# Kernel tuning notes

Hardware: AMD Instinct MI355X
Metric: run time of the kernel (lower is better)

The kernel has to match this reference:

```python
import jax, jax.numpy as jnp
import numpy as np

B, L, E, H, V, DT, C = 64, 80, 256, 256, 30000, 100, 4
D = 4 * L * H  # BatchNorm / FC feature dim = max_length * hidden * 4
EPS = 1e-5


def setup_inputs() -> dict:
    key = jax.random.key(0)
    ks = jax.random.split(key, 20)
    n = lambda k, shape, s: jax.random.normal(k, shape, jnp.float32) * s
    g = 1.0 / np.sqrt(H)  # pytorch LSTM init scale
    return {
        "arg1": jax.random.randint(ks[0], (B, L), 0, V, dtype=jnp.int32),
        "arg2": jax.random.randint(ks[1], (B, L), 0, V, dtype=jnp.int32),
        "seq_lengths": jnp.full((B,), L, dtype=jnp.int32),
        "transE1": jax.random.normal(ks[2], (L, DT), jnp.float32),
        "transE2": jax.random.normal(ks[3], (L, DT), jnp.float32),
        # learned parameters
        "table": n(ks[4], (V, E), 0.05),                 # embedding (xavier-ish)
        "Wih_f": n(ks[5], (4 * H, E), g),
        "Whh_f": n(ks[6], (4 * H, H), g),
        "bih_f": n(ks[7], (4 * H,), g),
        "bhh_f": n(ks[8], (4 * H,), g),
        "Wih_b": n(ks[9], (4 * H, E), g),
        "Whh_b": n(ks[10], (4 * H, H), g),
        "bih_b": n(ks[11], (4 * H,), g),
        "bhh_b": n(ks[12], (4 * H,), g),
        "R": jax.random.uniform(ks[13], (2 * E, 2 * E), jnp.float32),  # torch.rand init
        "gamma": jnp.ones((D,), jnp.float32),
        "beta": jnp.zeros((D,), jnp.float32),
        "fcW": n(ks[14], (C, D), 0.01),
        "fcb": jnp.zeros((C,), jnp.float32),
    }


def _lstm_dir(x, Wih, Whh, b):
    # x: (B, L, E); pytorch gate order i, f, g, o
    xg = jnp.einsum('ble,ge->blg', x, Wih) + b          # (B, L, 4H)
    xg = jnp.swapaxes(xg, 0, 1)                         # (L, B, 4H)
    h0 = jnp.zeros((x.shape[0], Whh.shape[1]), x.dtype)

    def step(carry, g_t):
        h, c = carry
        gates = g_t + h @ Whh.T
        i, f, gg, o = jnp.split(gates, 4, axis=-1)
        c = jax.nn.sigmoid(f) * c + jax.nn.sigmoid(i) * jnp.tanh(gg)
        h = jax.nn.sigmoid(o) * jnp.tanh(c)
        return (h, c), h

    _, hs = jax.lax.scan(step, (h0, h0), xg)
    return jnp.swapaxes(hs, 0, 1)                       # (B, L, H)


def _bilstm(x, Wih_f, Whh_f, bih_f, bhh_f, Wih_b, Whh_b, bih_b, bhh_b):
    fwd = _lstm_dir(x, Wih_f, Whh_f, bih_f + bhh_f)
    bwd = _lstm_dir(x[:, ::-1], Wih_b, Whh_b, bih_b + bhh_b)[:, ::-1]
    return jnp.concatenate([fwd, bwd], axis=-1)         # (B, L, 2H)


def _forward(arg1, arg2, transE1, transE2, table, Wih_f, Whh_f, bih_f, bhh_f,
             Wih_b, Whh_b, bih_b, bhh_b, R, gamma, beta, fcW, fcb):
    # deal_transE: relation[i,j] = tanh(mean(arg1_word_i - arg2_word_j));
    # identical for every batch element -> block-diagonal kron.
    m1 = transE1.mean(axis=1)                           # (L,)
    m2 = transE2.mean(axis=1)                           # (L,)
    rel = jnp.tanh(m1[:, None] - m2[None, :])           # (L, L)
    kg = jax.lax.stop_gradient(jnp.kron(jnp.eye(B, dtype=rel.dtype), rel))  # (B*L, B*L)

    e1 = table[arg1]                                    # (B, L, E); dropout p=0 -> identity
    e2 = table[arg2]
    o1 = _bilstm(e1, Wih_f, Whh_f, bih_f, bhh_f, Wih_b, Whh_b, bih_b, bhh_b)
    o2 = _bilstm(e2, Wih_f, Whh_f, bih_f, bhh_f, Wih_b, Whh_b, bih_b, bhh_b)

    N = B * L
    t1 = o1.reshape(N, 2 * H)
    t2 = o2.reshape(N, 2 * H)

    last = jnp.tanh((t1 @ R) @ t2.T) + kg               # (N, N)
    sf1 = jax.nn.softmax(last, axis=1).mean(axis=0)[:, None]  # (N, 1)
    sf2 = jax.nn.softmax(last, axis=0).mean(axis=1)[:, None]  # (N, 1)

    out1 = (t1 * sf2).reshape(B, L, 2 * H)
    out2 = (t2 * sf1).reshape(B, L, 2 * H)
    out = jnp.concatenate([out1, out2], axis=1).reshape(B, -1)  # (B, D)

    # BatchNorm1d in training mode (biased variance over batch)
    mu = out.mean(axis=0)
    var = out.var(axis=0)
    xn = (out - mu) / jnp.sqrt(var + EPS) * gamma + beta

    logits = xn @ fcW.T + fcb
    return jax.nn.log_softmax(logits, axis=1)           # (B, C)


def reference(arg1, arg2, seq_lengths, transE1, transE2, table, Wih_f, Whh_f,
              bih_f, bhh_f, Wih_b, Whh_b, bih_b, bhh_b, R, gamma, beta, fcW, fcb):
    del seq_lengths  # only encodes (B, L), which are static here
    return _forward(arg1, arg2, transE1, transE2, table, Wih_f, Whh_f, bih_f,
                    bhh_f, Wih_b, Whh_b, bih_b, bhh_b, R, gamma, beta, fcW, fcb)
```

## Files before the change

### kernel.cpp

```cpp
#include <hip/hip_runtime.h>
#include <cstddef>
#include <cstdint>

typedef unsigned short ushort_t;

constexpr int B_ = 64, L_ = 80, E_ = 256, H_ = 256, C_ = 4, DT_ = 100;
constexpr int N_ = B_ * L_;
constexpr int G4_ = 4 * H_;
constexpr int DH2_ = 2 * H_;
constexpr int DF_ = 4 * L_ * H_;
constexpr float EPS_ = 1e-5f;
constexpr int FB_USH = 8192;

typedef short s8v __attribute__((ext_vector_type(8)));
typedef float f4v __attribute__((ext_vector_type(4)));
typedef ushort_t us8 __attribute__((ext_vector_type(8)));

__device__ inline ushort_t f2bf_rn(float x) {
    uint32_t u = __builtin_bit_cast(uint32_t, x);
    uint32_t r = (u + 0x7fffu + ((u >> 16) & 1u)) >> 16;
    return (ushort_t)r;
}
__device__ inline float bf2f(ushort_t h) {
    uint32_t u = ((uint32_t)h) << 16;
    return __builtin_bit_cast(float, u);
}
__device__ inline float rcpf(float x) { return __builtin_amdgcn_rcpf(x); }
__device__ inline float sigm(float x) { return rcpf(1.f + __expf(-x)); }
__device__ inline float tanh_fast(float x) {
    float e2 = __expf(2.f * x);
    return 1.f - 2.f * rcpf(1.f + e2);
}

#define MFMA_B16(a, b, c) __builtin_amdgcn_mfma_f32_16x16x32_bf16((a), (b), (c), 0, 0, 0)

__global__ void k_rel(const float* __restrict__ tE1, const float* __restrict__ tE2,
                      float* __restrict__ rel) {
    __shared__ float m1[80], m2[80];
    int t = threadIdx.x;
    if (t < 80) {
        float s = 0.f;
        for (int k = 0; k < DT_; ++k) s += tE1[t * DT_ + k];
        m1[t] = s * (1.0f / DT_);
    } else if (t < 160) {
        int i = t - 80;
        float s = 0.f;
        for (int k = 0; k < DT_; ++k) s += tE2[i * DT_ + k];
        m2[i] = s * (1.0f / DT_);
    }
    __syncthreads();
    for (int idx = t; idx < 80 * 80; idx += blockDim.x)
        rel[idx] = tanhf(m1[idx / 80] - m2[idx % 80]);
}

__global__ void k_embed2(const int* __restrict__ arg1, const int* __restrict__ arg2,
                         const float* __restrict__ table,
                         ushort_t* __restrict__ ehi, ushort_t* __restrict__ elo) {
    int r = blockIdx.x;
    int rr = (r >= N_) ? (r - N_) : r;
    int idx = (r >= N_) ? arg2[rr] : arg1[rr];
    float v = table[(size_t)idx * E_ + threadIdx.x];
    ushort_t h = f2bf_rn(v);
    ehi[(size_t)r * E_ + threadIdx.x] = h;
    elo[(size_t)r * E_ + threadIdx.x] = f2bf_rn(v - bf2f(h));
}

__global__ void k_pack2(const float* __restrict__ Wih_f, const float* __restrict__ Wih_b,
                        const float* __restrict__ bih_f, const float* __restrict__ bhh_f,
                        const float* __restrict__ bih_b, const float* __restrict__ bhh_b,
                        const float* __restrict__ R,
                        ushort_t* __restrict__ Wchi, ushort_t* __restrict__ Wclo,
                        float* __restrict__ bcat,
                        ushort_t* __restrict__ Rthi, ushort_t* __restrict__ Rtlo) {
    int i = blockIdx.x * blockDim.x + threadIdx.x;
    if (i < 2 * G4_ * E_) {
        float v = (i < G4_ * E_) ? Wih_f[i] : Wih_b[i - G4_ * E_];
        ushort_t h = f2bf_rn(v);
        Wchi[i] = h;
        Wclo[i] = f2bf_rn(v - bf2f(h));
    }
    if (i < 2 * G4_)
        bcat[i] = (i < G4_) ? (bih_f[i] + bhh_f[i]) : (bih_b[i - G4_] + bhh_b[i - G4_]);
    if (i < 512 * 512) {
        int m = i >> 9, k = i & 511;
        float v = R[k * 512 + m];
        ushort_t h = f2bf_rn(v);
        Rthi[i] = h;
        Rtlo[i] = f2bf_rn(v - bf2f(h));
    }
}

__global__ void k_packw(const float* __restrict__ Whh_f, const float* __restrict__ Whh_b,
                        ushort_t* __restrict__ Bhi, ushort_t* __restrict__ Blo) {
    int idx = blockIdx.x * 256 + threadIdx.x;
    if (idx >= 2 * 16 * 8 * 4 * 64 * 8) return;
    int e = idx & 7;
    int lane = (idx >> 3) & 63;
    int g = (idx >> 9) & 3;
    int kt = (idx >> 11) & 7;
    int w = (idx >> 14) & 15;
    int d = idx >> 18;
    int c = lane & 15, q = lane >> 4;
    int row = g * 256 + w * 16 + c;
    int k = kt * 32 + q * 8 + e;
    const float* W = d ? Whh_b : Whh_f;
    float v = W[row * 256 + k];
    ushort_t hi = f2bf_rn(v);
    Bhi[idx] = hi;
    Blo[idx] = f2bf_rn(v - bf2f(hi));
}

__global__ void k_initlstm(ushort_t* __restrict__ fragbuf, int* __restrict__ flags) {
    int i = blockIdx.x * 256 + threadIdx.x;
    if (i < 256) flags[i] = 0;
    uint4* p = (uint4*)fragbuf;
    for (int jj = i; jj < 32768; jj += gridDim.x * 256)
        p[jj] = make_uint4(0u, 0u, 0u, 0u);
}

__global__ __launch_bounds__(256, 2) void k_lstm9(
        const float* __restrict__ xg,
        const ushort_t* __restrict__ Bhi, const ushort_t* __restrict__ Blo,
        float* __restrict__ o1, float* __restrict__ o2,
        ushort_t* __restrict__ o1hi, ushort_t* __restrict__ o1lo,
        ushort_t* __restrict__ o2hi, ushort_t* __restrict__ o2lo,
        ushort_t* __restrict__ fragbuf, int* __restrict__ flags) {
    const int bid = blockIdx.x;
    const int s = bid & 15;
    const int cg = (bid >> 4) & 7;
    const int d = bid >> 7;
    const int tid = threadIdx.x;
    const int g = tid >> 6, lane = tid & 63;
    const int c16 = lane & 15, qq = lane >> 4;

    __shared__ __align__(16) ushort_t Abuf[8192];
    __shared__ float pre[4][16][16];

    s8v bh[8], bl[8];
    {
        const s8v* BH = (const s8v*)Bhi;
        const s8v* BL = (const s8v*)Blo;
        int base = (d * 16 + s) * 2048 + g * 64 + lane;
        #pragma unroll
        for (int kt = 0; kt < 8; ++kt) {
            bh[kt] = BH[base + kt * 256];
            bl[kt] = BL[base + kt * 256];
        }
    }

    const int c_loc = tid >> 4, j = tid & 15;
    const int kglob = s * 16 + j;
    const int p_kt = kglob >> 5;
    const int p_q = (kglob & 31) >> 3, p_e = kglob & 7;
    const int p_lane = c_loc | (p_q << 4);
    const int fb_off = (p_kt * 64 + p_lane) * 8 + p_e;
    const int cc = cg * 16 + c_loc;
    const int w = cc >> 6, bb = cc & 63;
    float* o_out = w ? o2 : o1;
    ushort_t* ophi = w ? o2hi : o1hi;
    ushort_t* oplo = w ? o2lo : o1lo;
    float cst = 0.f;

    const int grp = bid >> 4;
    int* gflags = flags + grp * 16;
    const size_t fbbase = (size_t)grp * 2 * FB_USH;

    for (int t = 0; t < L_; ++t) {
        int l = d ? (L_ - 1 - t) : t;

        float xv[4];
        {
            const float* xp = xg + (size_t)(w * N_ + bb * L_ + l) * 2048
                              + d * 1024 + kglob;
            #pragma unroll
            for (int gg = 0; gg < 4; ++gg) xv[gg] = xp[gg * 256];
        }

        if (t > 0) {
            if (tid < 16) {
                while (__hip_atomic_load(&gflags[tid], __ATOMIC_RELAXED,
                                         __HIP_MEMORY_SCOPE_AGENT) < t)
                    __builtin_amdgcn_s_sleep(2);
            }
            __syncthreads();
        }

        {
            const unsigned long long* src = (const unsigned long long*)(fragbuf
                + fbbase + (size_t)(t & 1) * FB_USH);
            unsigned long long* dst = (unsigned long long*)Abuf;
            #pragma unroll
            for (int r = 0; r < 8; ++r)
                dst[r * 256 + tid] = __hip_atomic_load(
                    &src[r * 256 + tid], __ATOMIC_RELAXED,
                    __HIP_MEMORY_SCOPE_AGENT);
        }
        __syncthreads();

        f4v acc = {0.f, 0.f, 0.f, 0.f};
        {
            const s8v* AH = (const s8v*)&Abuf[0];
            const s8v* AL = (const s8v*)&Abuf[4096];
            #pragma unroll
            for (int kt = 0; kt < 8; ++kt) {
                s8v ah = AH[kt * 64 + lane];
                s8v al = AL[kt * 64 + lane];
                acc = MFMA_B16(ah, bh[kt], acc);
                acc = MFMA_B16(ah, bl[kt], acc);
                acc = MFMA_B16(al, bh[kt], acc);
            }
        }
        #pragma unroll
        for (int r = 0; r < 4; ++r)
            pre[g][qq * 4 + r][c16] = acc[r];
        __syncthreads();

        float h;
        ushort_t hh, hl;
        size_t oidx;
        {
            float pi = pre[0][c_loc][j] + xv[0];
            float pf = pre[1][c_loc][j] + xv[1];
            float pg = pre[2][c_loc][j] + xv[2];
            float po = pre[3][c_loc][j] + xv[3];
            float si = sigm(pi), sf_ = sigm(pf), so = sigm(po);
            cst = sf_ * cst + si * tanh_fast(pg);
            h = so * tanh_fast(cst);
            oidx = (size_t)(bb * L_ + l) * DH2_ + d * H_ + kglob;
            hh = f2bf_rn(h);
            hl = f2bf_rn(h - bf2f(hh));
            ushort_t* fbn = fragbuf + fbbase + (size_t)((t + 1) & 1) * FB_USH;
            __hip_atomic_store(&fbn[fb_off], hh, __ATOMIC_RELAXED,
                               __HIP_MEMORY_SCOPE_AGENT);
            __hip_atomic_store(&fbn[4096 + fb_off], hl, __ATOMIC_RELAXED,
                               __HIP_MEMORY_SCOPE_AGENT);
        }
        __syncthreads();

        if (tid == 0)
            __hip_atomic_store(&flags[bid], t + 1, __ATOMIC_RELAXED,
                               __HIP_MEMORY_SCOPE_AGENT);

        o_out[oidx] = h;
        ophi[oidx] = hh;
        oplo[oidx] = hl;
    }
}

__global__ __launch_bounds__(256) void k_gemm_bf(
        const ushort_t* __restrict__ Ahi, const ushort_t* __restrict__ Alo,
        const ushort_t* __restrict__ Bthi, const ushort_t* __restrict__ Btlo,
        const float* __restrict__ bias, float* __restrict__ Cout,
        ushort_t* __restrict__ Couthi, ushort_t* __restrict__ Coutlo,
        int M, int Nn, int K) {
    __shared__ ushort_t smpool[4][4096];
    const int tid = threadIdx.x;
    const int w = tid >> 6, lane = tid & 63;
    const int wr = w >> 1, wc = w & 1;
    const int c16 = lane & 15, q4 = lane >> 4;
    const int nbx = Nn >> 7;
    const int cpx = ((M >> 7) * nbx) >> 3;
    const int fid = blockIdx.x;
    const int swz = (fid & 7) * cpx + (fid >> 3);
    const int bx = swz % nbx, by = swz / nbx;
    const int r0 = by * 128, c0 = bx * 128;

    f4v acc[4][4] = {};
    const ushort_t* planes[4] = {
        Ahi + (size_t)r0 * K, Alo + (size_t)r0 * K,
        Bthi + (size_t)c0 * K, Btlo + (size_t)c0 * K };

    for (int kk = 0; kk < K; kk += 32) {
        #pragma unroll
        for (int p = 0; p < 4; ++p) {
            const ushort_t* src = planes[p] + kk;
            #pragma unroll
            for (int it = 0; it < 2; ++it) {
                int idx = it * 256 + tid;
                int row = idx >> 2, q = idx & 3;
                *(us8*)&smpool[p][(q * 128 + row) * 8] =
                    *(const us8*)&src[(size_t)row * K + q * 8];
            }
        }
        __syncthreads();
        s8v ah[4], al[4], bhv[4], blv[4];
        #pragma unroll
        for (int mi = 0; mi < 4; ++mi) {
            int ar = wr * 64 + mi * 16 + c16;
            ah[mi] = *(const s8v*)&smpool[0][(q4 * 128 + ar) * 8];
            al[mi] = *(const s8v*)&smpool[1][(q4 * 128 + ar) * 8];
        }
        #pragma unroll
        for (int ni = 0; ni < 4; ++ni) {
            int br = wc * 64 + ni * 16 + c16;
            bhv[ni] = *(const s8v*)&smpool[2][(q4 * 128 + br) * 8];
            blv[ni] = *(const s8v*)&smpool[3][(q4 * 128 + br) * 8];
        }
        #pragma unroll
        for (int mi = 0; mi < 4; ++mi)
            #pragma unroll
            for (int ni = 0; ni < 4; ++ni) {
                acc[mi][ni] = MFMA_B16(ah[mi], bhv[ni], acc[mi][ni]);
                acc[mi][ni] = MFMA_B16(ah[mi], blv[ni], acc[mi][ni]);
                acc[mi][ni] = MFMA_B16(al[mi], bhv[ni], acc[mi][ni]);
            }
        __syncthreads();
    }
    #pragma unroll
    for (int mi = 0; mi < 4; ++mi)
        #pragma unroll
        for (int rg = 0; rg < 4; ++rg) {
            int row = r0 + wr * 64 + mi * 16 + q4 * 4 + rg;
            #pragma unroll
            for (int ni = 0; ni < 4; ++ni) {
                int col = c0 + wc * 64 + ni * 16 + c16;
                float v = acc[mi][ni][rg] + (bias ? bias[col] : 0.f);
                size_t idx = (size_t)row * Nn + col;
                if (Couthi) {
                    ushort_t h = f2bf_rn(v);
                    Couthi[idx] = h;
                    Coutlo[idx] = f2bf_rn(v - bf2f(h));
                } else {
                    Cout[idx] = v;
                }
            }
        }
}

__global__ __launch_bounds__(256) void k_bigm(
        const ushort_t* __restrict__ uhi, const ushort_t* __restrict__ ulo,
        const ushort_t* __restrict__ vhi, const ushort_t* __restrict__ vlo,
        const float* __restrict__ rel, float* __restrict__ Ebuf,
        float* __restrict__ rowpart, float* __restrict__ colpart) {
    __shared__ ushort_t smpool[4][4096];
    const int tid = threadIdx.x;
    const int w = tid >> 6, lane = tid & 63;
    const int wr = w >> 1, wc = w & 1;
    const int c16 = lane & 15, q4 = lane >> 4;
    const int fid = blockIdx.x;
    const int swz = (fid & 7) * 200 + (fid >> 3);
    const int bx = swz % 40, by = swz / 40;
    const int r0 = by * 128, c0 = bx * 128;

    f4v acc[4][4] = {};
    const ushort_t* planes[4] = {
        uhi + (size_t)r0 * DH2_, ulo + (size_t)r0 * DH2_,
        vhi + (size_t)c0 * DH2_, vlo + (size_t)c0 * DH2_ };

    for (int kk = 0; kk < 16; ++kk) {
        #pragma unroll
        for (int p = 0; p < 4; ++p) {
            const ushort_t* src = planes[p] + kk * 32;
            #pragma unroll
            for (int it = 0; it < 2; ++it) {
                int idx = it * 256 + tid;
                int row = idx >> 2, q = idx & 3;
                *(us8*)&smpool[p][(q * 128 + row) * 8] =
                    *(const us8*)&src[(size_t)row * DH2_ + q * 8];
            }
        }
        __syncthreads();
        s8v ah[4], al[4], bhv[4], blv[4];
        #pragma unroll
        for (int mi = 0; mi < 4; ++mi) {
            int ar = wr * 64 + mi * 16 + c16;
            ah[mi] = *(const s8v*)&smpool[0][(q4 * 128 + ar) * 8];
            al[mi] = *(const s8v*)&smpool[1][(q4 * 128 + ar) * 8];
        }
        #pragma unroll
        for (int ni = 0; ni < 4; ++ni) {
            int br = wc * 64 + ni * 16 + c16;
            bhv[ni] = *(const s8v*)&smpool[2][(q4 * 128 + br) * 8];
            blv[ni] = *(const s8v*)&smpool[3][(q4 * 128 + br) * 8];
        }
        #pragma unroll
        for (int mi = 0; mi < 4; ++mi)
            #pragma unroll
            for (int ni = 0; ni < 4; ++ni) {
                acc[mi][ni] = MFMA_B16(ah[mi], bhv[ni], acc[mi][ni]);
                acc[mi][ni] = MFMA_B16(ah[mi], blv[ni], acc[mi][ni]);
                acc[mi][ni] = MFMA_B16(al[mi], bhv[ni], acc[mi][ni]);
            }
        __syncthreads();
    }

    float* rowred = (float*)&smpool[0][0];
    float* colred = rowred + 128 * 32;

    int gcolv[4], bjv[4], ljv[4];
    #pragma unroll
    for (int ni = 0; ni < 4; ++ni) {
        int coll = wc * 64 + ni * 16 + c16;
        gcolv[ni] = c0 + coll;
        bjv[ni] = gcolv[ni] / 80;
        ljv[ni] = gcolv[ni] - bjv[ni] * 80;
    }
    float csumv[4] = {0.f, 0.f, 0.f, 0.f};
    #pragma unroll
    for (int mi = 0; mi < 4; ++mi) {
        #pragma unroll
        for (int rg = 0; rg < 4; ++rg) {
            int rowl = wr * 64 + mi * 16 + q4 * 4 + rg;
            int grow = r0 + rowl;
            int bi = grow / 80, li = grow - bi * 80;
            float rsum = 0.f;
            #pragma unroll
            for (int ni = 0; ni < 4; ++ni) {
                float v = tanhf(acc[mi][ni][rg]);
                if (bi == bjv[ni]) v += rel[li * 80 + ljv[ni]];
                float ev = __expf(v);
                Ebuf[(size_t)grow * N_ + gcolv[ni]] = ev;
                rsum += ev;
                csumv[ni] += ev;
            }
            rowred[rowl * 32 + wc * 16 + c16] = rsum;
        }
    }
    #pragma unroll
    for (int ni = 0; ni < 4; ++ni) {
        int coll = wc * 64 + ni * 16 + c16;
        colred[coll * 8 + wr * 4 + q4] = csumv[ni];
    }
    __syncthreads();
    if (tid < 128) {
        float ssum = 0.f;
        #pragma unroll
        for (int t = 0; t < 32; ++t) ssum += rowred[tid * 32 + t];
        rowpart[(size_t)bx * N_ + r0 + tid] = ssum;
    } else {
        int c = tid - 128;
        float ssum = 0.f;
        #pragma unroll
        for (int t = 0; t < 8; ++t) ssum += colred[c * 8 + t];
        colpart[(size_t)by * N_ + c0 + c] = ssum;
    }
}

__global__ void k_redsum(const float* __restrict__ rowpart, const float* __restrict__ colpart,
                         float* __restrict__ rowinv, float* __restrict__ colinv) {
    int i = blockIdx.x * blockDim.x + threadIdx.x;
    if (i < N_) {
        float rs = 0.f, cs = 0.f;
        for (int t = 0; t < 40; ++t) {
            rs += rowpart[(size_t)t * N_ + i];
            cs += colpart[(size_t)t * N_ + i];
        }
        rowinv[i] = 1.f / rs;
        colinv[i] = 1.f / cs;
    }
}

__global__ __launch_bounds__(256) void k_sf2(const float* __restrict__ Ebuf,
                                             const float* __restrict__ colinv,
                                             float* __restrict__ sf2) {
    int i = blockIdx.x;
    float p = 0.f;
    for (int jj = threadIdx.x; jj < N_; jj += 256)
        p += Ebuf[(size_t)i * N_ + jj] * colinv[jj];
    __shared__ float red[256];
    red[threadIdx.x] = p;
    __syncthreads();
    for (int ss = 128; ss > 0; ss >>= 1) {
        if (threadIdx.x < ss) red[threadIdx.x] += red[threadIdx.x + ss];
        __syncthreads();
    }
    if (threadIdx.x == 0) sf2[i] = red[0] * (1.f / N_);
}

__global__ __launch_bounds__(256) void k_sf1part(const float* __restrict__ Ebuf,
                                                 const float* __restrict__ rowinv,
                                                 float* __restrict__ sf1part) {
    int col = blockIdx.x * 256 + threadIdx.x;
    int rc = blockIdx.y;
    float acc = 0.f;
    int r0 = rc * 320;
    for (int ii = 0; ii < 320; ++ii) {
        int row = r0 + ii;
        acc += Ebuf[(size_t)row * N_ + col] * rowinv[row];
    }
    sf1part[(size_t)rc * N_ + col] = acc;
}

__global__ void k_sf1red(const float* __restrict__ sf1part, float* __restrict__ sf1) {
    int jj = blockIdx.x * blockDim.x + threadIdx.x;
    if (jj < N_) {
        float s = 0.f;
        for (int t = 0; t < 16; ++t) s += sf1part[(size_t)t * N_ + jj];
        sf1[jj] = s * (1.f / N_);
    }
}

__global__ void k_bnstats(const float* __restrict__ o1, const float* __restrict__ o2,
                          const float* __restrict__ sf1, const float* __restrict__ sf2,
                          float* __restrict__ bnmu, float* __restrict__ bnrstd) {
    int f = blockIdx.x * 256 + threadIdx.x;
    int seg = f / (L_ * DH2_);
    int rem = f - seg * (L_ * DH2_);
    int l = rem >> 9, hh = rem & 511;
    const float* t = seg ? o2 : o1;
    const float* sf = seg ? sf1 : sf2;
    float s = 0.f, s2 = 0.f;
    for (int b = 0; b < B_; ++b) {
        int row = b * L_ + l;
        float x = t[(size_t)row * DH2_ + hh] * sf[row];
        s += x;
        s2 += x * x;
    }
    float mu = s * (1.f / B_);
    float v = fmaxf(s2 * (1.f / B_) - mu * mu, 0.f);
    bnmu[f] = mu;
    bnrstd[f] = rsqrtf(v + EPS_);
}

__global__ __launch_bounds__(256) void k_logits1(
        const float* __restrict__ o1, const float* __restrict__ o2,
        const float* __restrict__ sf1, const float* __restrict__ sf2,
        const float* __restrict__ bnmu, const float* __restrict__ bnrstd,
        const float* __restrict__ gamma, const float* __restrict__ beta,
        const float* __restrict__ fcW, float* __restrict__ part) {
    int b = blockIdx.x, ch = blockIdx.y;
    int tid = threadIdx.x;
    int f0 = ch * (DF_ / 5);
    float acc[4] = {0.f, 0.f, 0.f, 0.f};
    for (int f = f0 + tid; f < f0 + DF_ / 5; f += 256) {
        int seg = f / (L_ * DH2_);
        int rem = f - seg * (L_ * DH2_);
        int l = rem >> 9, hh = rem & 511;
        int row = b * L_ + l;
        float val = (seg ? o2 : o1)[(size_t)row * DH2_ + hh] * (seg ? sf1 : sf2)[row];
        float xn = (val - bnmu[f]) * bnrstd[f] * gamma[f] + beta[f];
        #pragma unroll
        for (int c = 0; c < 4; ++c) acc[c] += xn * fcW[(size_t)c * DF_ + f];
    }
    __shared__ float red[4][257];
    #pragma unroll
    for (int c = 0; c < 4; ++c) red[c][tid] = acc[c];
    __syncthreads();
    for (int ss = 128; ss > 0; ss >>= 1) {
        if (tid < ss)
            #pragma unroll
            for (int c = 0; c < 4; ++c) red[c][tid] += red[c][tid + ss];
        __syncthreads();
    }
    if (tid < 4) part[((size_t)b * 5 + ch) * 4 + tid] = red[tid][0];
}

__global__ void k_logits2(const float* __restrict__ part,
                          const float* __restrict__ fcb,
                          float* __restrict__ dout) {
    int b = blockIdx.x;
    if (threadIdx.x == 0) {
        float lg[4], mx = -1e30f;
        #pragma unroll
        for (int c = 0; c < 4; ++c) {
            float v = fcb[c];
            for (int ch = 0; ch < 5; ++ch) v += part[((size_t)b * 5 + ch) * 4 + c];
            lg[c] = v;
            mx = fmaxf(mx, v);
        }
        float se = 0.f;
        #pragma unroll
        for (int c = 0; c < 4; ++c) se += expf(lg[c] - mx);
        float lse = mx + logf(se);
        #pragma unroll
        for (int c = 0; c < 4; ++c) dout[b * 4 + c] = lg[c] - lse;
    }
}

extern "C" void kernel_launch(void* const* d_in, const int* in_sizes, int n_in,
                              void* d_out, int out_size, void* d_ws, size_t ws_size,
                              hipStream_t stream) {
    const int* arg1 = (const int*)d_in[0];
    const int* arg2 = (const int*)d_in[1];
    const float* tE1 = (const float*)d_in[3];
    const float* tE2 = (const float*)d_in[4];
    const float* table = (const float*)d_in[5];
    const float* Wih_f = (const float*)d_in[6];
    const float* Whh_f = (const float*)d_in[7];
    const float* bih_f = (const float*)d_in[8];
    const float* bhh_f = (const float*)d_in[9];
    const float* Wih_b = (const float*)d_in[10];
    const float* Whh_b = (const float*)d_in[11];
    const float* bih_b = (const float*)d_in[12];
    const float* bhh_b = (const float*)d_in[13];
    const float* R = (const float*)d_in[14];
    const float* gamma = (const float*)d_in[15];
    const float* beta = (const float*)d_in[16];
    const float* fcW = (const float*)d_in[17];
    const float* fcb = (const float*)d_in[18];
    float* dout = (float*)d_out;

    float* ws = (float*)d_ws;
    size_t off = 0;
    auto alloc = [&](size_t n) { float* p = ws + off; off += n; return p; };

    constexpr size_t PL = (size_t)N_ * DH2_;

    float* rel = alloc(80 * 80);
    float* eplanes = alloc((size_t)2 * N_ * E_);
    float* Wcplanes = alloc((size_t)2 * G4_ * E_);
    float* bcat = alloc(2 * G4_);
    float* Rtplanes = alloc((size_t)262144);
    float* o1 = alloc(PL);
    float* o2 = alloc(PL);
    float* planesA = alloc(PL);
    float* planesU = alloc(PL);
    float* rowpart = alloc((size_t)40 * N_);
    float* colpart = alloc((size_t)40 * N_);
    float* rowinv = alloc(N_);
    float* colinv = alloc(N_);
    float* sf1part = alloc((size_t)16 * N_);
    float* sf1 = alloc(N_);
    float* sf2 = alloc(N_);
    float* bnmu = alloc(DF_);
    float* bnrstd = alloc(DF_);
    float* lgpart = alloc((size_t)B_ * 5 * 4);
    ushort_t* Bhi = (ushort_t*)alloc(262144);
    ushort_t* Blo = (ushort_t*)alloc(262144);
    ushort_t* fragbuf = (ushort_t*)alloc(131072);
    int* flags = (int*)alloc(256);
    float* xg = alloc((size_t)N_ * N_);
    float* Ebuf = xg;

    ushort_t* ehi = (ushort_t*)eplanes;
    ushort_t* elo = ehi + (size_t)2 * N_ * E_;
    ushort_t* Wchi = (ushort_t*)Wcplanes;
    ushort_t* Wclo = Wchi + (size_t)2 * G4_ * E_;
    ushort_t* Rthi = (ushort_t*)Rtplanes;
    ushort_t* Rtlo = Rthi + 512 * 512;
    ushort_t* o1hi = (ushort_t*)planesA;
    ushort_t* o1lo = o1hi + PL;
    ushort_t* uhi = (ushort_t*)planesU;
    ushort_t* ulo = uhi + PL;
    ushort_t* o2hi = ehi;
    ushort_t* o2lo = elo;

    k_rel<<<1, 256, 0, stream>>>(tE1, tE2, rel);
    k_embed2<<<2 * N_, 256, 0, stream>>>(arg1, arg2, table, ehi, elo);
    k_pack2<<<2048, 256, 0, stream>>>(Wih_f, Wih_b, bih_f, bhh_f, bih_b, bhh_b, R,
                                      Wchi, Wclo, bcat, Rthi, Rtlo);
    k_packw<<<2048, 256, 0, stream>>>(Whh_f, Whh_b, Bhi, Blo);
    k_initlstm<<<64, 256, 0, stream>>>(fragbuf, flags);
    k_gemm_bf<<<1280, 256, 0, stream>>>(
        ehi, elo, Wchi, Wclo, bcat, xg, nullptr, nullptr, 2 * N_, 2048, E_);
    k_lstm9<<<256, 256, 0, stream>>>(xg, Bhi, Blo, o1, o2,
                                     o1hi, o1lo, o2hi, o2lo, fragbuf, flags);
    k_gemm_bf<<<160, 256, 0, stream>>>(
        o1hi, o1lo, Rthi, Rtlo, nullptr, nullptr, uhi, ulo, N_, 512, 512);
    k_bigm<<<1600, 256, 0, stream>>>(
        uhi, ulo, o2hi, o2lo, rel, Ebuf, rowpart, colpart);
    k_redsum<<<(N_ + 255) / 256, 256, 0, stream>>>(rowpart, colpart, rowinv, colinv);
    k_sf2<<<N_, 256, 0, stream>>>(Ebuf, colinv, sf2);
    k_sf1part<<<dim3(20, 16), 256, 0, stream>>>(Ebuf, rowinv, sf1part);
    k_sf1red<<<(N_ + 255) / 256, 256, 0, stream>>>(sf1part, sf1);
    k_bnstats<<<DF_ / 256, 256, 0, stream>>>(o1, o2, sf1, sf2, bnmu, bnrstd);
    k_logits1<<<dim3(B_, 5), 256, 0, stream>>>(o1, o2, sf1, sf2, bnmu, bnrstd,
                                               gamma, beta, fcW, lgpart);
    k_logits2<<<B_, 64, 0, stream>>>(lgpart, fcb, dout);
}
```

Before: 639.0 us.

## Fuse prep kernels, store exp matrix as bf16, merge softmax passes, drop fp32 LSTM outputs

Five small prep kernels are merged into one launch. The N×N exponential matrix is stored as bf16 instead of fp32, which halves its write and read traffic, and the row and column softmax weighting passes are merged into one read of it. The LSTM no longer writes fp32 outputs; downstream kernels rebuild values from the hi/lo bf16 planes. The LSTM spin-wait now polls per wavefront without a block barrier and with a shorter sleep, which risks ordering and visibility problems, and bf16 rounding of the exponentials adds error.

```diff
diff --git a/kernel.cpp b/kernel.cpp
--- a/kernel.cpp
+++ b/kernel.cpp
@@ -34,94 +34,91 @@
 
 #define MFMA_B16(a, b, c) __builtin_amdgcn_mfma_f32_16x16x32_bf16((a), (b), (c), 0, 0, 0)
 
-__global__ void k_rel(const float* __restrict__ tE1, const float* __restrict__ tE2,
-                      float* __restrict__ rel) {
+__global__ void k_prep(const int* __restrict__ arg1, const int* __restrict__ arg2,
+                       const float* __restrict__ table,
+                       const float* __restrict__ tE1, const float* __restrict__ tE2,
+                       const float* __restrict__ Wih_f, const float* __restrict__ Wih_b,
+                       const float* __restrict__ bih_f, const float* __restrict__ bhh_f,
+                       const float* __restrict__ bih_b, const float* __restrict__ bhh_b,
+                       const float* __restrict__ R,
+                       const float* __restrict__ Whh_f, const float* __restrict__ Whh_b,
+                       ushort_t* __restrict__ ehi, ushort_t* __restrict__ elo,
+                       ushort_t* __restrict__ Wchi, ushort_t* __restrict__ Wclo,
+                       float* __restrict__ bcat,
+                       ushort_t* __restrict__ Rthi, ushort_t* __restrict__ Rtlo,
+                       ushort_t* __restrict__ Bhi, ushort_t* __restrict__ Blo,
+                       ushort_t* __restrict__ fragbuf, int* __restrict__ flags,
+                       float* __restrict__ rel) {
     __shared__ float m1[80], m2[80];
-    int t = threadIdx.x;
-    if (t < 80) {
-        float s = 0.f;
-        for (int k = 0; k < DT_; ++k) s += tE1[t * DT_ + k];
-        m1[t] = s * (1.0f / DT_);
-    } else if (t < 160) {
-        int i = t - 80;
-        float s = 0.f;
-        for (int k = 0; k < DT_; ++k) s += tE2[i * DT_ + k];
-        m2[i] = s * (1.0f / DT_);
-    }
-    __syncthreads();
-    for (int idx = t; idx < 80 * 80; idx += blockDim.x)
-        rel[idx] = tanhf(m1[idx / 80] - m2[idx % 80]);
-}
-
-__global__ void k_embed2(const int* __restrict__ arg1, const int* __restrict__ arg2,
-                         const float* __restrict__ table,
-                         ushort_t* __restrict__ ehi, ushort_t* __restrict__ elo) {
-    int r = blockIdx.x;
-    int rr = (r >= N_) ? (r - N_) : r;
-    int idx = (r >= N_) ? arg2[rr] : arg1[rr];
-    float v = table[(size_t)idx * E_ + threadIdx.x];
-    ushort_t h = f2bf_rn(v);
-    ehi[(size_t)r * E_ + threadIdx.x] = h;
-    elo[(size_t)r * E_ + threadIdx.x] = f2bf_rn(v - bf2f(h));
-}
-
-__global__ void k_pack2(const float* __restrict__ Wih_f, const float* __restrict__ Wih_b,
-                        const float* __restrict__ bih_f, const float* __restrict__ bhh_f,
-                        const float* __restrict__ bih_b, const float* __restrict__ bhh_b,
-                        const float* __restrict__ R,
-                        ushort_t* __restrict__ Wchi, ushort_t* __restrict__ Wclo,
-                        float* __restrict__ bcat,
-                        ushort_t* __restrict__ Rthi, ushort_t* __restrict__ Rtlo) {
-    int i = blockIdx.x * blockDim.x + threadIdx.x;
-    if (i < 2 * G4_ * E_) {
-        float v = (i < G4_ * E_) ? Wih_f[i] : Wih_b[i - G4_ * E_];
+    int blk = blockIdx.x;
+    int tid = threadIdx.x;
+    if (blk < 10240) {
+        int r = blk;
+        int rr = (r >= N_) ? (r - N_) : r;
+        int idx = (r >= N_) ? arg2[rr] : arg1[rr];
+        float v = table[(size_t)idx * E_ + tid];
         ushort_t h = f2bf_rn(v);
-        Wchi[i] = h;
-        Wclo[i] = f2bf_rn(v - bf2f(h));
-    }
-    if (i < 2 * G4_)
-        bcat[i] = (i < G4_) ? (bih_f[i] + bhh_f[i]) : (bih_b[i - G4_] + bhh_b[i - G4_]);
-    if (i < 512 * 512) {
-        int m = i >> 9, k = i & 511;
-        float v = R[k * 512 + m];
-        ushort_t h = f2bf_rn(v);
-        Rthi[i] = h;
-        Rtlo[i] = f2bf_rn(v - bf2f(h));
-    }
-}
-
-__global__ void k_packw(const float* __restrict__ Whh_f, const float* __restrict__ Whh_b,
-                        ushort_t* __restrict__ Bhi, ushort_t* __restrict__ Blo) {
-    int idx = blockIdx.x * 256 + threadIdx.x;
-    if (idx >= 2 * 16 * 8 * 4 * 64 * 8) return;
-    int e = idx & 7;
-    int lane = (idx >> 3) & 63;
-    int g = (idx >> 9) & 3;
-    int kt = (idx >> 11) & 7;
-    int w = (idx >> 14) & 15;
-    int d = idx >> 18;
-    int c = lane & 15, q = lane >> 4;
-    int row = g * 256 + w * 16 + c;
-    int k = kt * 32 + q * 8 + e;
-    const float* W = d ? Whh_b : Whh_f;
-    float v = W[row * 256 + k];
-    ushort_t hi = f2bf_rn(v);
-    Bhi[idx] = hi;
-    Blo[idx] = f2bf_rn(v - bf2f(hi));
-}
-
-__global__ void k_initlstm(ushort_t* __restrict__ fragbuf, int* __restrict__ flags) {
-    int i = blockIdx.x * 256 + threadIdx.x;
-    if (i < 256) flags[i] = 0;
-    uint4* p = (uint4*)fragbuf;
-    for (int jj = i; jj < 32768; jj += gridDim.x * 256)
-        p[jj] = make_uint4(0u, 0u, 0u, 0u);
-}
-
-__global__ __launch_bounds__(256, 2) void k_lstm9(
+        ehi[(size_t)r * E_ + tid] = h;
+        elo[(size_t)r * E_ + tid] = f2bf_rn(v - bf2f(h));
+    } else if (blk < 12288) {
+        int i = (blk - 10240) * 256 + tid;
+        if (i < 2 * G4_ * E_) {
+            float v = (i < G4_ * E_) ? Wih_f[i] : Wih_b[i - G4_ * E_];
+            ushort_t h = f2bf_rn(v);
+            Wchi[i] = h;
+            Wclo[i] = f2bf_rn(v - bf2f(h));
+        }
+        if (i < 2 * G4_)
+            bcat[i] = (i < G4_) ? (bih_f[i] + bhh_f[i]) : (bih_b[i - G4_] + bhh_b[i - G4_]);
+        if (i < 512 * 512) {
+            int m = i >> 9, k = i & 511;
+            float v = R[k * 512 + m];
+            ushort_t h = f2bf_rn(v);
+            Rthi[i] = h;
+            Rtlo[i] = f2bf_rn(v - bf2f(h));
+        }
+    } else if (blk < 14336) {
+        int idx = (blk - 12288) * 256 + tid;
+        int e = idx & 7;
+        int lane = (idx >> 3) & 63;
+        int g = (idx >> 9) & 3;
+        int kt = (idx >> 11) & 7;
+        int w = (idx >> 14) & 15;
+        int d = idx >> 18;
+        int c = lane & 15, q = lane >> 4;
+        int row = g * 256 + w * 16 + c;
+        int k = kt * 32 + q * 8 + e;
+        const float* W = d ? Whh_b : Whh_f;
+        float v = W[row * 256 + k];
+        ushort_t hi = f2bf_rn(v);
+        Bhi[idx] = hi;
+        Blo[idx] = f2bf_rn(v - bf2f(hi));
+    } else if (blk < 14400) {
+        int i = (blk - 14336) * 256 + tid;
+        if (i < 256) flags[i] = 0;
+        uint4* p = (uint4*)fragbuf;
+        for (int jj = i; jj < 32768; jj += 64 * 256)
+            p[jj] = make_uint4(0u, 0u, 0u, 0u);
+    } else {
+        if (tid < 80) {
+            float s = 0.f;
+            for (int k = 0; k < DT_; ++k) s += tE1[tid * DT_ + k];
+            m1[tid] = s * (1.0f / DT_);
+        } else if (tid < 160) {
+            int i = tid - 80;
+            float s = 0.f;
+            for (int k = 0; k < DT_; ++k) s += tE2[i * DT_ + k];
+            m2[i] = s * (1.0f / DT_);
+        }
+        __syncthreads();
+        for (int idx = tid; idx < 80 * 80; idx += 256)
+            rel[idx] = tanhf(m1[idx / 80] - m2[idx % 80]);
+    }
+}
+
+__global__ __launch_bounds__(256, 2) void k_lstm9b(
         const float* __restrict__ xg,
         const ushort_t* __restrict__ Bhi, const ushort_t* __restrict__ Blo,
-        float* __restrict__ o1, float* __restrict__ o2,
         ushort_t* __restrict__ o1hi, ushort_t* __restrict__ o1lo,
         ushort_t* __restrict__ o2hi, ushort_t* __restrict__ o2lo,
         ushort_t* __restrict__ fragbuf, int* __restrict__ flags) {
@@ -156,7 +153,6 @@
     const int fb_off = (p_kt * 64 + p_lane) * 8 + p_e;
     const int cc = cg * 16 + c_loc;
     const int w = cc >> 6, bb = cc & 63;
-    float* o_out = w ? o2 : o1;
     ushort_t* ophi = w ? o2hi : o1hi;
     ushort_t* oplo = w ? o2lo : o1lo;
     float cst = 0.f;
@@ -177,12 +173,11 @@
         }
 
         if (t > 0) {
-            if (tid < 16) {
-                while (__hip_atomic_load(&gflags[tid], __ATOMIC_RELAXED,
+            if (lane < 16) {
+                while (__hip_atomic_load(&gflags[lane], __ATOMIC_RELAXED,
                                          __HIP_MEMORY_SCOPE_AGENT) < t)
-                    __builtin_amdgcn_s_sleep(2);
-            }
-            __syncthreads();
+                    __builtin_amdgcn_s_sleep(1);
+            }
         }
 
         {
@@ -215,7 +210,6 @@
             pre[g][qq * 4 + r][c16] = acc[r];
         __syncthreads();
 
-        float h;
         ushort_t hh, hl;
         size_t oidx;
         {
@@ -225,7 +219,7 @@
             float po = pre[3][c_loc][j] + xv[3];
             float si = sigm(pi), sf_ = sigm(pf), so = sigm(po);
             cst = sf_ * cst + si * tanh_fast(pg);
-            h = so * tanh_fast(cst);
+            float h = so * tanh_fast(cst);
             oidx = (size_t)(bb * L_ + l) * DH2_ + d * H_ + kglob;
             hh = f2bf_rn(h);
             hl = f2bf_rn(h - bf2f(hh));
@@ -241,7 +235,6 @@
             __hip_atomic_store(&flags[bid], t + 1, __ATOMIC_RELAXED,
                                __HIP_MEMORY_SCOPE_AGENT);
 
-        o_out[oidx] = h;
         ophi[oidx] = hh;
         oplo[oidx] = hl;
     }
@@ -330,7 +323,7 @@
 __global__ __launch_bounds__(256) void k_bigm(
         const ushort_t* __restrict__ uhi, const ushort_t* __restrict__ ulo,
         const ushort_t* __restrict__ vhi, const ushort_t* __restrict__ vlo,
-        const float* __restrict__ rel, float* __restrict__ Ebuf,
+        const float* __restrict__ rel, ushort_t* __restrict__ Ebf,
         float* __restrict__ rowpart, float* __restrict__ colpart) {
     __shared__ ushort_t smpool[4][4096];
     const int tid = threadIdx.x;
@@ -408,10 +401,11 @@
             for (int ni = 0; ni < 4; ++ni) {
                 float v = tanhf(acc[mi][ni][rg]);
                 if (bi == bjv[ni]) v += rel[li * 80 + ljv[ni]];
-                float ev = __expf(v);
-                Ebuf[(size_t)grow * N_ + gcolv[ni]] = ev;
-                rsum += ev;
-                csumv[ni] += ev;
+                ushort_t eb = f2bf_rn(__expf(v));
+                Ebf[(size_t)grow * N_ + gcolv[ni]] = eb;
+                float er = bf2f(eb);
+                rsum += er;
+                csumv[ni] += er;
             }
             rowred[rowl * 32 + wc * 16 + c16] = rsum;
         }
@@ -450,59 +444,67 @@
     }
 }
 
-__global__ __launch_bounds__(256) void k_sf2(const float* __restrict__ Ebuf,
-                                             const float* __restrict__ colinv,
-                                             float* __restrict__ sf2) {
-    int i = blockIdx.x;
-    float p = 0.f;
-    for (int jj = threadIdx.x; jj < N_; jj += 256)
-        p += Ebuf[(size_t)i * N_ + jj] * colinv[jj];
-    __shared__ float red[256];
-    red[threadIdx.x] = p;
-    __syncthreads();
-    for (int ss = 128; ss > 0; ss >>= 1) {
-        if (threadIdx.x < ss) red[threadIdx.x] += red[threadIdx.x + ss];
-        __syncthreads();
-    }
-    if (threadIdx.x == 0) sf2[i] = red[0] * (1.f / N_);
-}
-
-__global__ __launch_bounds__(256) void k_sf1part(const float* __restrict__ Ebuf,
-                                                 const float* __restrict__ rowinv,
-                                                 float* __restrict__ sf1part) {
-    int col = blockIdx.x * 256 + threadIdx.x;
-    int rc = blockIdx.y;
-    float acc = 0.f;
-    int r0 = rc * 320;
+__global__ __launch_bounds__(256) void k_sfpass(
+        const ushort_t* __restrict__ Ebf,
+        const float* __restrict__ rowinv, const float* __restrict__ colinv,
+        float* __restrict__ sf1part, float* __restrict__ sf2part) {
+    const int tid = threadIdx.x;
+    const int lane = tid & 63, wv = tid >> 6;
+    const int col = blockIdx.x * 256 + tid;
+    const int rc = blockIdx.y;
+    const int r0 = rc * 320;
+    __shared__ float rowp4[320][4];
+
+    float cinv = colinv[col];
+    float accC = 0.f;
+    #pragma unroll 4
     for (int ii = 0; ii < 320; ++ii) {
         int row = r0 + ii;
-        acc += Ebuf[(size_t)row * N_ + col] * rowinv[row];
-    }
-    sf1part[(size_t)rc * N_ + col] = acc;
-}
-
-__global__ void k_sf1red(const float* __restrict__ sf1part, float* __restrict__ sf1) {
-    int jj = blockIdx.x * blockDim.x + threadIdx.x;
-    if (jj < N_) {
-        float s = 0.f;
-        for (int t = 0; t < 16; ++t) s += sf1part[(size_t)t * N_ + jj];
-        sf1[jj] = s * (1.f / N_);
-    }
-}
-
-__global__ void k_bnstats(const float* __restrict__ o1, const float* __restrict__ o2,
+        float e = bf2f(Ebf[(size_t)row * N_ + col]);
+        accC += e * rowinv[row];
+        float t2 = e * cinv;
+        #pragma unroll
+        for (int off = 32; off > 0; off >>= 1) t2 += __shfl_down(t2, off, 64);
+        if (lane == 0) rowp4[ii][wv] = t2;
+    }
+    sf1part[(size_t)rc * N_ + col] = accC;
+    __syncthreads();
+    if (tid < 320) {
+        float s = rowp4[tid][0] + rowp4[tid][1] + rowp4[tid][2] + rowp4[tid][3];
+        sf2part[(size_t)blockIdx.x * N_ + r0 + tid] = s;
+    }
+}
+
+__global__ void k_sfred(const float* __restrict__ sf1part,
+                        const float* __restrict__ sf2part,
+                        float* __restrict__ sf1, float* __restrict__ sf2) {
+    int j = blockIdx.x * blockDim.x + threadIdx.x;
+    if (j < N_) {
+        float s1 = 0.f;
+        for (int t = 0; t < 16; ++t) s1 += sf1part[(size_t)t * N_ + j];
+        sf1[j] = s1 * (1.f / N_);
+        float s2 = 0.f;
+        for (int t = 0; t < 20; ++t) s2 += sf2part[(size_t)t * N_ + j];
+        sf2[j] = s2 * (1.f / N_);
+    }
+}
+
+__global__ void k_bnstats(const ushort_t* __restrict__ o1hi, const ushort_t* __restrict__ o1lo,
+                          const ushort_t* __restrict__ o2hi, const ushort_t* __restrict__ o2lo,
                           const float* __restrict__ sf1, const float* __restrict__ sf2,
                           float* __restrict__ bnmu, float* __restrict__ bnrstd) {
     int f = blockIdx.x * 256 + threadIdx.x;
     int seg = f / (L_ * DH2_);
     int rem = f - seg * (L_ * DH2_);
     int l = rem >> 9, hh = rem & 511;
-    const float* t = seg ? o2 : o1;
+    const ushort_t* phi = seg ? o2hi : o1hi;
+    const ushort_t* plo = seg ? o2lo : o1lo;
     const float* sf = seg ? sf1 : sf2;
     float s = 0.f, s2 = 0.f;
     for (int b = 0; b < B_; ++b) {
         int row = b * L_ + l;
-        float x = t[(size_t)row * DH2_ + hh] * sf[row];
+        size_t idx = (size_t)row * DH2_ + hh;
+        float x = (bf2f(phi[idx]) + bf2f(plo[idx])) * sf[row];
         s += x;
         s2 += x * x;
     }
@@ -513,7 +515,8 @@
 }
 
 __global__ __launch_bounds__(256) void k_logits1(
-        const float* __restrict__ o1, const float* __restrict__ o2,
+        const ushort_t* __restrict__ o1hi, const ushort_t* __restrict__ o1lo,
+        const ushort_t* __restrict__ o2hi, const ushort_t* __restrict__ o2lo,
         const float* __restrict__ sf1, const float* __restrict__ sf2,
         const float* __restrict__ bnmu, const float* __restrict__ bnrstd,
         const float* __restrict__ gamma, const float* __restrict__ beta,
@@ -527,7 +530,10 @@
         int rem = f - seg * (L_ * DH2_);
         int l = rem >> 9, hh = rem & 511;
         int row = b * L_ + l;
-        float val = (seg ? o2 : o1)[(size_t)row * DH2_ + hh] * (seg ? sf1 : sf2)[row];
+        size_t idx = (size_t)row * DH2_ + hh;
+        const ushort_t* phi = seg ? o2hi : o1hi;
+        const ushort_t* plo = seg ? o2lo : o1lo;
+        float val = (bf2f(phi[idx]) + bf2f(plo[idx])) * (seg ? sf1 : sf2)[row];
         float xn = (val - bnmu[f]) * bnrstd[f] * gamma[f] + beta[f];
         #pragma unroll
         for (int c = 0; c < 4; ++c) acc[c] += xn * fcW[(size_t)c * DF_ + f];
@@ -601,8 +607,6 @@
     float* Wcplanes = alloc((size_t)2 * G4_ * E_);
     float* bcat = alloc(2 * G4_);
     float* Rtplanes = alloc((size_t)262144);
-    float* o1 = alloc(PL);
-    float* o2 = alloc(PL);
     float* planesA = alloc(PL);
     float* planesU = alloc(PL);
     float* rowpart = alloc((size_t)40 * N_);
@@ -610,6 +614,7 @@
     float* rowinv = alloc(N_);
     float* colinv = alloc(N_);
     float* sf1part = alloc((size_t)16 * N_);
+    float* sf2part = alloc((size_t)20 * N_);
     float* sf1 = alloc(N_);
     float* sf2 = alloc(N_);
     float* bnmu = alloc(DF_);
@@ -620,7 +625,7 @@
     ushort_t* fragbuf = (ushort_t*)alloc(131072);
     int* flags = (int*)alloc(256);
     float* xg = alloc((size_t)N_ * N_);
-    float* Ebuf = xg;
+    ushort_t* Ebf = (ushort_t*)xg;
 
     ushort_t* ehi = (ushort_t*)eplanes;
     ushort_t* elo = ehi + (size_t)2 * N_ * E_;
@@ -635,26 +640,25 @@
     ushort_t* o2hi = ehi;
     ushort_t* o2lo = elo;
 
-    k_rel<<<1, 256, 0, stream>>>(tE1, tE2, rel);
-    k_embed2<<<2 * N_, 256, 0, stream>>>(arg1, arg2, table, ehi, elo);
-    k_pack2<<<2048, 256, 0, stream>>>(Wih_f, Wih_b, bih_f, bhh_f, bih_b, bhh_b, R,
-                                      Wchi, Wclo, bcat, Rthi, Rtlo);
-    k_packw<<<2048, 256, 0, stream>>>(Whh_f, Whh_b, Bhi, Blo);
-    k_initlstm<<<64, 256, 0, stream>>>(fragbuf, flags);
+    k_prep<<<14401, 256, 0, stream>>>(arg1, arg2, table, tE1, tE2,
+                                      Wih_f, Wih_b, bih_f, bhh_f, bih_b, bhh_b,
+                                      R, Whh_f, Whh_b,
+                                      ehi, elo, Wchi, Wclo, bcat, Rthi, Rtlo,
+                                      Bhi, Blo, fragbuf, flags, rel);
     k_gemm_bf<<<1280, 256, 0, stream>>>(
         ehi, elo, Wchi, Wclo, bcat, xg, nullptr, nullptr, 2 * N_, 2048, E_);
-    k_lstm9<<<256, 256, 0, stream>>>(xg, Bhi, Blo, o1, o2,
-                                     o1hi, o1lo, o2hi, o2lo, fragbuf, flags);
+    k_lstm9b<<<256, 256, 0, stream>>>(xg, Bhi, Blo,
+                                      o1hi, o1lo, o2hi, o2lo, fragbuf, flags);
     k_gemm_bf<<<160, 256, 0, stream>>>(
         o1hi, o1lo, Rthi, Rtlo, nullptr, nullptr, uhi, ulo, N_, 512, 512);
     k_bigm<<<1600, 256, 0, stream>>>(
-        uhi, ulo, o2hi, o2lo, rel, Ebuf, rowpart, colpart);
+        uhi, ulo, o2hi, o2lo, rel, Ebf, rowpart, colpart);
     k_redsum<<<(N_ + 255) / 256, 256, 0, stream>>>(rowpart, colpart, rowinv, colinv);
-    k_sf2<<<N_, 256, 0, stream>>>(Ebuf, colinv, sf2);
-    k_sf1part<<<dim3(20, 16), 256, 0, stream>>>(Ebuf, rowinv, sf1part);
-    k_sf1red<<<(N_ + 255) / 256, 256, 0, stream>>>(sf1part, sf1);
-    k_bnstats<<<DF_ / 256, 256, 0, stream>>>(o1, o2, sf1, sf2, bnmu, bnrstd);
-    k_logits1<<<dim3(B_, 5), 256, 0, stream>>>(o1, o2, sf1, sf2, bnmu, bnrstd,
-                                               gamma, beta, fcW, lgpart);
+    k_sfpass<<<dim3(20, 16), 256, 0, stream>>>(Ebf, rowinv, colinv, sf1part, sf2part);
+    k_sfred<<<(N_ + 255) / 256, 256, 0, stream>>>(sf1part, sf2part, sf1, sf2);
+    k_bnstats<<<DF_ / 256, 256, 0, stream>>>(o1hi, o1lo, o2hi, o2lo, sf1, sf2,
+                                             bnmu, bnrstd);
+    k_logits1<<<dim3(B_, 5), 256, 0, stream>>>(o1hi, o1lo, o2hi, o2lo, sf1, sf2,
+                                               bnmu, bnrstd, gamma, beta, fcW, lgpart);
     k_logits2<<<B_, 64, 0, stream>>>(lgpart, fcb, dout);
 }
```

Measured after the change: 744.1 us. +16.4%, slower.
